# Kernel optimization log

Hardware: AMD Instinct MI355X
Metric: run time of the kernel (lower is better)

The kernel has to match this reference:

```python
import jax, jax.numpy as jnp
import numpy as np

N, E, IN, H, OUT = 100000, 1200000, 128, 64, 2
L = 3          # num GCN layers
EPS = 1e-5     # BatchNorm eps


def setup_inputs() -> dict:
    key = jax.random.key(0)
    ks = jax.random.split(key, 14)
    x = jax.random.normal(ks[0], (N, IN), dtype=jnp.float32)
    edge_index = jax.random.randint(ks[1], (2, E), 0, N, dtype=jnp.int64)
    # GCNConv weights (glorot-ish scale) and biases
    w0 = jax.random.normal(ks[2], (IN, H), dtype=jnp.float32) / np.float32(np.sqrt(IN))
    w1 = jax.random.normal(ks[3], (H, H), dtype=jnp.float32) / np.float32(np.sqrt(H))
    w2 = jax.random.normal(ks[4], (H, H), dtype=jnp.float32) / np.float32(np.sqrt(H))
    biases = jax.random.normal(ks[5], (L, H), dtype=jnp.float32) * 0.01
    # BatchNorm (eval mode): gamma, beta, running mean/var per layer
    gamma = jnp.ones((L, H), jnp.float32) + 0.1 * jax.random.normal(ks[6], (L, H), dtype=jnp.float32)
    beta = 0.1 * jax.random.normal(ks[7], (L, H), dtype=jnp.float32)
    run_mean = 0.1 * jax.random.normal(ks[8], (L, H), dtype=jnp.float32)
    run_var = 0.5 + jax.random.uniform(ks[9], (L, H), dtype=jnp.float32)  # strictly positive
    # classifier
    cls_w = jax.random.normal(ks[10], (H, OUT), dtype=jnp.float32) / np.float32(np.sqrt(H))
    cls_b = jnp.zeros((OUT,), jnp.float32)
    return {"x": x, "edge_index": edge_index, "w0": w0, "w1": w1, "w2": w2,
            "biases": biases, "gamma": gamma, "beta": beta,
            "run_mean": run_mean, "run_var": run_var,
            "cls_w": cls_w, "cls_b": cls_b}


def reference(x, edge_index, w0, w1, w2, biases, gamma, beta, run_mean, run_var, cls_w, cls_b):
    n = x.shape[0]
    loop = jnp.arange(n, dtype=edge_index.dtype)
    row = jnp.concatenate([edge_index[0], loop])  # source (with self-loops)
    col = jnp.concatenate([edge_index[1], loop])  # target (with self-loops)
    # symmetric normalization: D^{-1/2} (A+I) D^{-1/2}, degree on target index
    deg = jax.ops.segment_sum(jnp.ones(row.shape, x.dtype), col, num_segments=n)
    dinv = jnp.where(deg > 0, jax.lax.rsqrt(deg), 0.0)
    norm = dinv[row] * dinv[col]  # [E+N]

    h = x
    for l, w in enumerate((w0, w1, w2)):
        h = h @ w                                                   # [N,H]
        msg = norm[:, None] * h[row]                                # gather + scale [E+N,H]
        h = jax.ops.segment_sum(msg, col, num_segments=n) + biases[l]
        # BatchNorm1d (eval) + ReLU
        scale = gamma[l] * jax.lax.rsqrt(run_var[l] + EPS)
        h = jax.nn.relu((h - run_mean[l]) * scale + beta[l])
        # dropout is identity in eval mode
    return h @ cls_w + cls_b  # [N, OUT]
```

## Files before the change

### kernel.cpp

```cpp
#include <hip/hip_runtime.h>
#include <hip/hip_fp16.h>

#define EPS 1e-5f
#define ABITS 8
#define NBKT_MAX 512
#define ACHUNK 2048
#define BCAP 4096
#define BCSR 6144
#define CSHIFT 13
#define NCHUNK 16

typedef _Float16 half8 __attribute__((ext_vector_type(8)));
typedef float floatx4 __attribute__((ext_vector_type(4)));


__global__ __launch_bounds__(256) void bucketA_kernel(const int* __restrict__ ei, int E,
                                                      int* __restrict__ bucket_fill, unsigned* __restrict__ tmp) {
    __shared__ int2 edg[ACHUNK];
    __shared__ int hist[NBKT_MAX], lbase[NBKT_MAX], lcur[NBKT_MAX];
    int t = threadIdx.x;
    for (int i = t; i < NBKT_MAX; i += 256) { hist[i] = 0; lcur[i] = 0; }
    __syncthreads();
    int e0 = blockIdx.x * ACHUNK;
    int e1 = e0 + ACHUNK; if (e1 > E) e1 = E;
    int ne = e1 - e0;
    for (int idx = t; idx < ne; idx += 256) {
        int r = ei[e0 + idx], c = ei[E + e0 + idx];
        edg[idx] = make_int2(r, c);
        atomicAdd(&hist[c >> ABITS], 1);
    }
    __syncthreads();
    for (int i = t; i < NBKT_MAX; i += 256) {
        int h = hist[i];
        if (h) lbase[i] = atomicAdd(&bucket_fill[i], h);
    }
    __syncthreads();
    for (int idx = t; idx < ne; idx += 256) {
        int2 e = edg[idx];
        int b = e.y >> ABITS;
        int l = atomicAdd(&lcur[b], 1);
        tmp[(size_t)b * BCAP + lbase[b] + l] = ((unsigned)(e.y & 255) << 17) | (unsigned)e.x;
    }
}

__global__ __launch_bounds__(256) void bucketB_kernel(const unsigned* __restrict__ tmp,
                                                      const int* __restrict__ bucket_fill,
                                                      int2* __restrict__ rowse, float* __restrict__ dinv,
                                                      int* __restrict__ csr, int* __restrict__ perm, int n) {
    __shared__ unsigned edg[BCAP];
    __shared__ int cnt2[256 * NCHUNK];
    __shared__ int wsum[4];
    __shared__ int ccnt[16], cbaseS[16];
    int b = blockIdx.x, t = threadIdx.x;
    int lane = t & 63, wv = t >> 6;
    int n0 = b << ABITS;
    int cntN = n - n0; if (cntN > 256) cntN = 256;
    int ne = bucket_fill[b]; if (ne > BCAP) ne = BCAP;
    int base = b * BCAP;
    int cbase = b * BCSR;
    if (t < 16) ccnt[t] = 0;
    for (int i = t; i < 256 * NCHUNK; i += 256) cnt2[i] = 0;
    for (int idx = t; idx < ne; idx += 256) edg[idx] = tmp[(size_t)base + idx];
    __syncthreads();
    for (int idx = t; idx < ne; idx += 256) {
        unsigned e = edg[idx];
        int dstOff = e >> 17, src = e & 0x1FFFF;
        atomicAdd(&cnt2[dstOff * NCHUNK + (src >> CSHIFT)], 1);
    }
    __syncthreads();
    int c0 = 0;
#pragma unroll
    for (int c = 0; c < NCHUNK; ++c) c0 += cnt2[t * NCHUNK + c];
    int k0c = (c0 + 7) >> 3; if (k0c > 15) k0c = 15;
    int rank0 = 0;
    if (t < cntN) rank0 = atomicAdd(&ccnt[k0c], 1);
    int p0 = (c0 + 7) & ~7;
    int v = p0;
#pragma unroll
    for (int off = 1; off < 64; off <<= 1) {
        int u = __shfl_up(v, off);
        if (lane >= off) v += u;
    }
    if (lane == 63) wsum[wv] = v;
    __syncthreads();
    int addv = 0;
    for (int j = 0; j < wv; ++j) addv += wsum[j];
    int excl = v + addv - p0;
    int st0 = cbase + excl;
    if (t < cntN) {
        rowse[n0 + t] = make_int2(st0, st0 + c0);
        dinv[n0 + t] = rsqrtf((float)(c0 + 1));
        for (int j = c0; j < p0; ++j) csr[st0 + j] = n0 + t;
    }
    int run = st0;
#pragma unroll
    for (int c = 0; c < NCHUNK; ++c) {
        int vv = cnt2[t * NCHUNK + c];
        cnt2[t * NCHUNK + c] = run;
        run += vv;
    }
    if (t < 16) {
        int sacc = 0;
        for (int j = 0; j < t; ++j) sacc += ccnt[j];
        cbaseS[t] = sacc;
    }
    __syncthreads();
    if (t < cntN) perm[n0 + cbaseS[k0c] + rank0] = n0 + t;
    for (int idx = t; idx < ne; idx += 256) {
        unsigned e = edg[idx];
        int dstOff = e >> 17, src = e & 0x1FFFF;
        int key = dstOff * NCHUNK + (src >> CSHIFT);
        int pos = atomicAdd(&cnt2[key], 1);
        csr[pos] = src;
    }
}


template <int K, typename TIN>
__global__ __launch_bounds__(256) void gemm_kernel(const TIN* __restrict__ A, const float* __restrict__ W,
                                                   const float* __restrict__ dinv, __half* __restrict__ out, int n) {
    const int KP = K + 8;
    __shared__ _Float16 Ah[64 * (K + 8)];
    __shared__ _Float16 Wt[64 * (K + 8)];
    int tid = threadIdx.x;

    for (int idx = tid; idx < K * 64; idx += 256) {
        int k = idx >> 6, c = idx & 63;
        Wt[c * KP + k] = (_Float16)W[idx];
    }
    int row0 = blockIdx.x * 64;
    const TIN* Ab = A + (size_t)row0 * K;
    int limit = (n - row0) * K; if (limit > 64 * K) limit = 64 * K;

    if constexpr (sizeof(TIN) == 4) {
        for (int f = tid * 4; f < 64 * K; f += 1024) {
            float4 v = make_float4(0.f, 0.f, 0.f, 0.f);
            if (f + 3 < limit) {
                v = *(const float4*)((const float*)Ab + f);
            } else {
                if (f + 0 < limit) v.x = ((const float*)Ab)[f + 0];
                if (f + 1 < limit) v.y = ((const float*)Ab)[f + 1];
                if (f + 2 < limit) v.z = ((const float*)Ab)[f + 2];
            }
            int row = f / K, k = f % K;
            _Float16* dst = Ah + row * KP + k;
            dst[0] = (_Float16)v.x; dst[1] = (_Float16)v.y;
            dst[2] = (_Float16)v.z; dst[3] = (_Float16)v.w;
        }
    } else {
        for (int f = tid * 8; f < 64 * K; f += 2048) {
            uint4 v = make_uint4(0, 0, 0, 0);
            if (f + 7 < limit) {
                v = *(const uint4*)((const __half*)Ab + f);
            } else {
                const __half* hp = (const __half*)Ab;
                __half tmp8[8];
                for (int j = 0; j < 8; ++j) tmp8[j] = (f + j < limit) ? hp[f + j] : __half(0);
                v = *(const uint4*)tmp8;
            }
            int row = f / K, k = f % K;
            *(uint4*)(Ah + row * KP + k) = v;
        }
    }
    __syncthreads();

    int w = tid >> 6, lane = tid & 63;
    int m = lane & 15, quad = lane >> 4;
    const _Float16* Aw = Ah + (size_t)(w * 16 + m) * KP + quad * 8;
    const _Float16* Bw = Wt + (size_t)m * KP + quad * 8;

    floatx4 acc0 = {0.f, 0.f, 0.f, 0.f}, acc1 = acc0, acc2 = acc0, acc3 = acc0;
    for (int k0 = 0; k0 < K; k0 += 32) {
        half8 a  = *(const half8*)(Aw + k0);
        half8 b0 = *(const half8*)(Bw + 0 * 16 * KP + k0);
        half8 b1 = *(const half8*)(Bw + 1 * 16 * KP + k0);
        half8 b2 = *(const half8*)(Bw + 2 * 16 * KP + k0);
        half8 b3 = *(const half8*)(Bw + 3 * 16 * KP + k0);
        acc0 = __builtin_amdgcn_mfma_f32_16x16x32_f16(a, b0, acc0, 0, 0, 0);
        acc1 = __builtin_amdgcn_mfma_f32_16x16x32_f16(a, b1, acc1, 0, 0, 0);
        acc2 = __builtin_amdgcn_mfma_f32_16x16x32_f16(a, b2, acc2, 0, 0, 0);
        acc3 = __builtin_amdgcn_mfma_f32_16x16x32_f16(a, b3, acc3, 0, 0, 0);
    }

    int rbase = row0 + w * 16 + quad * 4;
#pragma unroll
    for (int r = 0; r < 4; ++r) {
        int row = rbase + r;
        if (row < n) {
            float dv = dinv[row];
            __half* o = out + (size_t)row * 64 + m;
            o[0]  = __float2half(acc0[r] * dv);
            o[16] = __float2half(acc1[r] * dv);
            o[32] = __float2half(acc2[r] * dv);
            o[48] = __float2half(acc3[r] * dv);
        }
    }
}


__device__ __forceinline__ void agg_add8(float4& lo, float4& hi, uint4 raw) {
    float2 p0 = __half22float2(*(const __half2*)&raw.x);
    float2 p1 = __half22float2(*(const __half2*)&raw.y);
    float2 p2 = __half22float2(*(const __half2*)&raw.z);
    float2 p3 = __half22float2(*(const __half2*)&raw.w);
    lo.x += p0.x; lo.y += p0.y; lo.z += p1.x; lo.w += p1.y;
    hi.x += p2.x; hi.y += p2.y; hi.z += p3.x; hi.w += p3.y;
}

__device__ __forceinline__ void agg_core(const __half* __restrict__ t, const float* __restrict__ dinv,
                                         const int2* __restrict__ rowse, const int* __restrict__ csr,
                                         const float* __restrict__ bias, const float* __restrict__ gamma,
                                         const float* __restrict__ beta, const float* __restrict__ mean,
                                         const float* __restrict__ var,
                                         int i, int fl, float4& resL, float4& resH, float& di) {
    uint4 self = *(const uint4*)(t + (size_t)i * 64 + fl * 8);

    float4 lo = make_float4(0.f, 0.f, 0.f, 0.f);
    float4 hi = make_float4(0.f, 0.f, 0.f, 0.f);

    int2 se = rowse[i];
    int deg = se.y - se.x;
    int padEnd = se.x + ((deg + 7) & ~7);
    for (int e = se.x; e < padEnd; e += 8) {
        int s0 = csr[e + 0], s1 = csr[e + 1], s2 = csr[e + 2], s3 = csr[e + 3];
        int s4 = csr[e + 4], s5 = csr[e + 5], s6 = csr[e + 6], s7 = csr[e + 7];
        uint4 r0 = *(const uint4*)(t + (size_t)s0 * 64 + fl * 8);
        uint4 r1 = *(const uint4*)(t + (size_t)s1 * 64 + fl * 8);
        uint4 r2 = *(const uint4*)(t + (size_t)s2 * 64 + fl * 8);
        uint4 r3 = *(const uint4*)(t + (size_t)s3 * 64 + fl * 8);
        uint4 r4 = *(const uint4*)(t + (size_t)s4 * 64 + fl * 8);
        uint4 r5 = *(const uint4*)(t + (size_t)s5 * 64 + fl * 8);
        uint4 r6 = *(const uint4*)(t + (size_t)s6 * 64 + fl * 8);
        uint4 r7 = *(const uint4*)(t + (size_t)s7 * 64 + fl * 8);
        agg_add8(lo, hi, r0); agg_add8(lo, hi, r1); agg_add8(lo, hi, r2); agg_add8(lo, hi, r3);
        agg_add8(lo, hi, r4); agg_add8(lo, hi, r5); agg_add8(lo, hi, r6); agg_add8(lo, hi, r7);
    }

    float coef = 1.0f - (float)(padEnd - se.y);
    {
        float2 p0 = __half22float2(*(const __half2*)&self.x);
        float2 p1 = __half22float2(*(const __half2*)&self.y);
        float2 p2 = __half22float2(*(const __half2*)&self.z);
        float2 p3 = __half22float2(*(const __half2*)&self.w);
        lo.x += coef * p0.x; lo.y += coef * p0.y; lo.z += coef * p1.x; lo.w += coef * p1.y;
        hi.x += coef * p2.x; hi.y += coef * p2.y; hi.z += coef * p3.x; hi.w += coef * p3.y;
    }

    di = dinv[i];
    lo.x *= di; lo.y *= di; lo.z *= di; lo.w *= di;
    hi.x *= di; hi.y *= di; hi.z *= di; hi.w *= di;

    float4 bbL = ((const float4*)bias)[2 * fl],  bbH = ((const float4*)bias)[2 * fl + 1];
    float4 ggL = ((const float4*)gamma)[2 * fl], ggH = ((const float4*)gamma)[2 * fl + 1];
    float4 beL = ((const float4*)beta)[2 * fl],  beH = ((const float4*)beta)[2 * fl + 1];
    float4 mmL = ((const float4*)mean)[2 * fl],  mmH = ((const float4*)mean)[2 * fl + 1];
    float4 vvL = ((const float4*)var)[2 * fl],   vvH = ((const float4*)var)[2 * fl + 1];
    resL.x = fmaxf((lo.x + bbL.x - mmL.x) * (ggL.x * rsqrtf(vvL.x + EPS)) + beL.x, 0.f);
    resL.y = fmaxf((lo.y + bbL.y - mmL.y) * (ggL.y * rsqrtf(vvL.y + EPS)) + beL.y, 0.f);
    resL.z = fmaxf((lo.z + bbL.z - mmL.z) * (ggL.z * rsqrtf(vvL.z + EPS)) + beL.z, 0.f);
    resL.w = fmaxf((lo.w + bbL.w - mmL.w) * (ggL.w * rsqrtf(vvL.w + EPS)) + beL.w, 0.f);
    resH.x = fmaxf((hi.x + bbH.x - mmH.x) * (ggH.x * rsqrtf(vvH.x + EPS)) + beH.x, 0.f);
    resH.y = fmaxf((hi.y + bbH.y - mmH.y) * (ggH.y * rsqrtf(vvH.y + EPS)) + beH.y, 0.f);
    resH.z = fmaxf((hi.z + bbH.z - mmH.z) * (ggH.z * rsqrtf(vvH.z + EPS)) + beH.z, 0.f);
    resH.w = fmaxf((hi.w + bbH.w - mmH.w) * (ggH.w * rsqrtf(vvH.w + EPS)) + beH.w, 0.f);
}

__global__ __launch_bounds__(256, 4) void agg_gemm_kernel(
        const __half* __restrict__ t, const float* __restrict__ dinv,
        const int2* __restrict__ rowse, const int* __restrict__ csr,
        const int* __restrict__ perm,
        const float* __restrict__ bias, const float* __restrict__ gamma,
        const float* __restrict__ beta, const float* __restrict__ mean,
        const float* __restrict__ var,
        const float* __restrict__ W,
        __half* __restrict__ tout, int n) {
    const int KP = 72;
    __shared__ _Float16 Ah[32 * 72];
    __shared__ _Float16 Wt[64 * 72];
    __shared__ int   nidS[32];
    __shared__ float dvS[32];

    int tid = threadIdx.x;
    for (int idx = tid; idx < 64 * 64; idx += 256) {
        int k = idx >> 6, c = idx & 63;
        Wt[c * KP + k] = (_Float16)W[idx];
    }

    int wave = tid >> 6, lane = tid & 63;
    int g = lane >> 3, fl = lane & 7;
    int slotInBlk = wave * 8 + g;
    int slot = blockIdx.x * 32 + slotInBlk;
    bool act = slot < n;

    if (act) {
        int i = perm[slot];
        float4 resL, resH; float di;
        agg_core(t, dinv, rowse, csr, bias, gamma, beta, mean, var, i, fl, resL, resH, di);
        __half2 h0 = __floats2half2_rn(resL.x, resL.y);
        __half2 h1 = __floats2half2_rn(resL.z, resL.w);
        __half2 h2 = __floats2half2_rn(resH.x, resH.y);
        __half2 h3 = __floats2half2_rn(resH.z, resH.w);
        uint4 pk;
        pk.x = *(unsigned*)&h0; pk.y = *(unsigned*)&h1;
        pk.z = *(unsigned*)&h2; pk.w = *(unsigned*)&h3;
        *(uint4*)(Ah + slotInBlk * KP + fl * 8) = pk;
        if (fl == 0) { nidS[slotInBlk] = i; dvS[slotInBlk] = di; }
    } else {
        uint4 z = make_uint4(0, 0, 0, 0);
        *(uint4*)(Ah + slotInBlk * KP + fl * 8) = z;
        if (fl == 0) { nidS[slotInBlk] = 0; dvS[slotInBlk] = 0.f; }
    }
    __syncthreads();

    int m = lane & 15, quad = lane >> 4;
    int mrow = (wave & 1) * 16;
    int c0 = (wave >> 1) * 32;
    const _Float16* Aw = Ah + (mrow + m) * KP + quad * 8;
    const _Float16* Bw = Wt + (c0 + m) * KP + quad * 8;

    floatx4 acc0 = {0.f, 0.f, 0.f, 0.f}, acc1 = acc0;
#pragma unroll
    for (int k0 = 0; k0 < 64; k0 += 32) {
        half8 a  = *(const half8*)(Aw + k0);
        half8 b0 = *(const half8*)(Bw + k0);
        half8 b1 = *(const half8*)(Bw + 16 * KP + k0);
        acc0 = __builtin_amdgcn_mfma_f32_16x16x32_f16(a, b0, acc0, 0, 0, 0);
        acc1 = __builtin_amdgcn_mfma_f32_16x16x32_f16(a, b1, acc1, 0, 0, 0);
    }
    __syncthreads();

#pragma unroll
    for (int r = 0; r < 4; ++r) {
        int row = mrow + quad * 4 + r;
        float dv = dvS[row];
        Ah[row * KP + c0 + m]      = (_Float16)(acc0[r] * dv);
        Ah[row * KP + c0 + 16 + m] = (_Float16)(acc1[r] * dv);
    }
    __syncthreads();

    if (act) {
        int node = nidS[slotInBlk];
        uint4 v = *(const uint4*)(Ah + slotInBlk * KP + fl * 8);
        *(uint4*)(tout + (size_t)node * 64 + fl * 8) = v;
    }
}

__global__ __launch_bounds__(256, 4) void agg_cls_kernel(
        const __half* __restrict__ t, const float* __restrict__ dinv,
        const int2* __restrict__ rowse, const int* __restrict__ csr,
        const int* __restrict__ perm,
        const float* __restrict__ bias, const float* __restrict__ gamma,
        const float* __restrict__ beta, const float* __restrict__ mean,
        const float* __restrict__ var,
        float* __restrict__ fout,
        const float* __restrict__ cls_w, const float* __restrict__ cls_b,
        int n) {
    int wave = threadIdx.x >> 6;
    int lane = threadIdx.x & 63;
    int g = lane >> 3;
    int fl = lane & 7;
    int slot = (blockIdx.x * (blockDim.x >> 6) + wave) * 8 + g;
    if (slot >= n) return;
    int i = perm[slot];

    float4 resL, resH; float di;
    agg_core(t, dinv, rowse, csr, bias, gamma, beta, mean, var, i, fl, resL, resH, di);

    const float4* cw = (const float4*)cls_w;
    float4 cwA = cw[4 * fl + 0], cwB = cw[4 * fl + 1], cwC = cw[4 * fl + 2], cwD = cw[4 * fl + 3];
    float c0 = resL.x * cwA.x + resL.y * cwA.z + resL.z * cwB.x + resL.w * cwB.z
             + resH.x * cwC.x + resH.y * cwC.z + resH.z * cwD.x + resH.w * cwD.z;
    float c1 = resL.x * cwA.y + resL.y * cwA.w + resL.z * cwB.y + resL.w * cwB.w
             + resH.x * cwC.y + resH.y * cwC.w + resH.z * cwD.y + resH.w * cwD.w;
    for (int off = 4; off > 0; off >>= 1) {
        c0 += __shfl_xor(c0, off);
        c1 += __shfl_xor(c1, off);
    }
    if (fl == 0) {
        fout[(size_t)i * 2 + 0] = c0 + cls_b[0];
        fout[(size_t)i * 2 + 1] = c1 + cls_b[1];
    }
}


extern "C" void kernel_launch(void* const* d_in, const int* in_sizes, int n_in,
                              void* d_out, int out_size, void* d_ws, size_t ws_size,
                              hipStream_t stream) {
    const float* x      = (const float*)d_in[0];
    const int*   ei     = (const int*)d_in[1];
    const float* w0     = (const float*)d_in[2];
    const float* w1     = (const float*)d_in[3];
    const float* w2     = (const float*)d_in[4];
    const float* biases = (const float*)d_in[5];
    const float* gamma  = (const float*)d_in[6];
    const float* beta   = (const float*)d_in[7];
    const float* rmean  = (const float*)d_in[8];
    const float* rvar   = (const float*)d_in[9];
    const float* cls_w  = (const float*)d_in[10];
    const float* cls_b  = (const float*)d_in[11];
    float* out = (float*)d_out;

    const int IN = 128, H = 64;
    const int N = in_sizes[0] / IN;
    const int E = in_sizes[1] / 2;

    char* p = (char*)d_ws;
    auto carve = [&](size_t bytes) { void* q = (void*)p; p += (bytes + 255) & ~(size_t)255; return q; };
    float* dinv    = (float*)carve((size_t)N * 4);
    int2*  rowse   = (int2*)carve((size_t)N * 8);
    int*   bucket_fill = (int*)carve((size_t)NBKT_MAX * 4);
    int*   perm    = (int*)carve((size_t)N * 4);
    unsigned* tmp  = (unsigned*)carve((size_t)NBKT_MAX * BCAP * 4);
    int*   csr     = (int*)carve((size_t)NBKT_MAX * BCSR * 4);
    __half* tA     = (__half*)carve((size_t)N * H * 2);
    __half* tB     = (__half*)carve((size_t)N * H * 2);

    int nbuckets = (N + (1 << ABITS) - 1) >> ABITS;
    int na = (E + ACHUNK - 1) / ACHUNK;

    hipMemsetAsync(bucket_fill, 0, (size_t)NBKT_MAX * 4, stream);
    bucketA_kernel<<<na, 256, 0, stream>>>(ei, E, bucket_fill, tmp);
    bucketB_kernel<<<nbuckets, 256, 0, stream>>>(tmp, bucket_fill, rowse, dinv, csr, perm, N);

    int gemm_grid = (N + 63) / 64;
    int agg_grid  = (N + 31) / 32;

    gemm_kernel<128, float><<<gemm_grid, 256, 0, stream>>>(x, w0, dinv, tA, N);
    agg_gemm_kernel<<<agg_grid, 256, 0, stream>>>(tA, dinv, rowse, csr, perm,
        biases + 0, gamma + 0, beta + 0, rmean + 0, rvar + 0, w1, tB, N);
    agg_gemm_kernel<<<agg_grid, 256, 0, stream>>>(tB, dinv, rowse, csr, perm,
        biases + H, gamma + H, beta + H, rmean + H, rvar + H, w2, tA, N);
    agg_cls_kernel<<<agg_grid, 256, 0, stream>>>(tA, dinv, rowse, csr, perm,
        biases + 2 * H, gamma + 2 * H, beta + 2 * H, rmean + 2 * H, rvar + 2 * H,
        out, cls_w, cls_b, N);
}
```

Before: 250.3 us.

## Merge all GCN stages into one persistent cooperative kernel with grid syncs

Replaces the six separate kernel launches (two bucketing passes, input GEMM, two aggregate+GEMM layers, final aggregate+classifier) with a single cooperative persistent kernel. Blocks loop over tiles within each phase and separate the phases with grid.sync, using one dynamic shared-memory buffer carved per phase. This removes per-launch overhead and the gaps between kernels. In exchange, occupancy is capped by the largest shared-memory phase, each block's loop adds extra __syncthreads, and every grid-wide barrier waits for the slowest block.

```diff
diff --git a/kernel.cpp b/kernel.cpp
--- a/kernel.cpp
+++ b/kernel.cpp
@@ -1,5 +1,8 @@
 #include <hip/hip_runtime.h>
 #include <hip/hip_fp16.h>
+#include <hip/hip_cooperative_groups.h>
+
+namespace cg = cooperative_groups;
 
 #define EPS 1e-5f
 #define ABITS 8
@@ -9,58 +12,72 @@
 #define BCSR 6144
 #define CSHIFT 13
 #define NCHUNK 16
+#define SMEM_BYTES 34816
 
 typedef _Float16 half8 __attribute__((ext_vector_type(8)));
 typedef float floatx4 __attribute__((ext_vector_type(4)));
 
-
-__global__ __launch_bounds__(256) void bucketA_kernel(const int* __restrict__ ei, int E,
-                                                      int* __restrict__ bucket_fill, unsigned* __restrict__ tmp) {
-    __shared__ int2 edg[ACHUNK];
-    __shared__ int hist[NBKT_MAX], lbase[NBKT_MAX], lcur[NBKT_MAX];
+struct GcnParams {
+    const float* x; const int* ei;
+    const float* w0; const float* w1; const float* w2;
+    const float* biases; const float* gamma; const float* beta;
+    const float* rmean; const float* rvar;
+    const float* cls_w; const float* cls_b;
+    float* out;
+    float* dinv; int2* rowse; int* bucket_fill; int* perm;
+    unsigned* tmp; int* csr; __half* tA; __half* tB;
+    int N, E, na, nbuckets, gtiles, atiles;
+};
+
+
+__device__ __forceinline__ void bucketA_body(char* smem, const GcnParams& P, int chunk) {
+    int2* edg  = (int2*)smem;
+    int* hist  = (int*)(smem + 16384);
+    int* lbase = (int*)(smem + 18432);
+    int* lcur  = (int*)(smem + 20480);
     int t = threadIdx.x;
     for (int i = t; i < NBKT_MAX; i += 256) { hist[i] = 0; lcur[i] = 0; }
     __syncthreads();
-    int e0 = blockIdx.x * ACHUNK;
-    int e1 = e0 + ACHUNK; if (e1 > E) e1 = E;
+    int e0 = chunk * ACHUNK;
+    int e1 = e0 + ACHUNK; if (e1 > P.E) e1 = P.E;
     int ne = e1 - e0;
     for (int idx = t; idx < ne; idx += 256) {
-        int r = ei[e0 + idx], c = ei[E + e0 + idx];
+        int r = P.ei[e0 + idx], c = P.ei[P.E + e0 + idx];
         edg[idx] = make_int2(r, c);
         atomicAdd(&hist[c >> ABITS], 1);
     }
     __syncthreads();
     for (int i = t; i < NBKT_MAX; i += 256) {
         int h = hist[i];
-        if (h) lbase[i] = atomicAdd(&bucket_fill[i], h);
+        if (h) lbase[i] = atomicAdd(&P.bucket_fill[i], h);
     }
     __syncthreads();
     for (int idx = t; idx < ne; idx += 256) {
         int2 e = edg[idx];
         int b = e.y >> ABITS;
         int l = atomicAdd(&lcur[b], 1);
-        tmp[(size_t)b * BCAP + lbase[b] + l] = ((unsigned)(e.y & 255) << 17) | (unsigned)e.x;
-    }
-}
-
-__global__ __launch_bounds__(256) void bucketB_kernel(const unsigned* __restrict__ tmp,
-                                                      const int* __restrict__ bucket_fill,
-                                                      int2* __restrict__ rowse, float* __restrict__ dinv,
-                                                      int* __restrict__ csr, int* __restrict__ perm, int n) {
-    __shared__ unsigned edg[BCAP];
-    __shared__ int cnt2[256 * NCHUNK];
-    __shared__ int wsum[4];
-    __shared__ int ccnt[16], cbaseS[16];
-    int b = blockIdx.x, t = threadIdx.x;
+        P.tmp[(size_t)b * BCAP + lbase[b] + l] = ((unsigned)(e.y & 255) << 17) | (unsigned)e.x;
+    }
+    __syncthreads();
+}
+
+
+__device__ __forceinline__ void bucketB_body(char* smem, const GcnParams& P, int b) {
+    unsigned* edg = (unsigned*)smem;
+    int* cnt2   = (int*)(smem + 16384);
+    int* wsum   = (int*)(smem + 32768);
+    int* ccnt   = (int*)(smem + 32784);
+    int* cbaseS = (int*)(smem + 32848);
+    int t = threadIdx.x;
     int lane = t & 63, wv = t >> 6;
     int n0 = b << ABITS;
-    int cntN = n - n0; if (cntN > 256) cntN = 256;
-    int ne = bucket_fill[b]; if (ne > BCAP) ne = BCAP;
+    int cntN = P.N - n0; if (cntN > 256) cntN = 256;
+    int ne = P.bucket_fill[b]; if (ne > BCAP) ne = BCAP;
     int base = b * BCAP;
     int cbase = b * BCSR;
     if (t < 16) ccnt[t] = 0;
     for (int i = t; i < 256 * NCHUNK; i += 256) cnt2[i] = 0;
-    for (int idx = t; idx < ne; idx += 256) edg[idx] = tmp[(size_t)base + idx];
+    for (int idx = t; idx < ne; idx += 256) edg[idx] = P.tmp[(size_t)base + idx];
     __syncthreads();
     for (int idx = t; idx < ne; idx += 256) {
         unsigned e = edg[idx];
@@ -88,9 +105,9 @@
     int excl = v + addv - p0;
     int st0 = cbase + excl;
     if (t < cntN) {
-        rowse[n0 + t] = make_int2(st0, st0 + c0);
-        dinv[n0 + t] = rsqrtf((float)(c0 + 1));
-        for (int j = c0; j < p0; ++j) csr[st0 + j] = n0 + t;
+        P.rowse[n0 + t] = make_int2(st0, st0 + c0);
+        P.dinv[n0 + t] = rsqrtf((float)(c0 + 1));
+        for (int j = c0; j < p0; ++j) P.csr[st0 + j] = n0 + t;
     }
     int run = st0;
 #pragma unroll
@@ -105,95 +122,78 @@
         cbaseS[t] = sacc;
     }
     __syncthreads();
-    if (t < cntN) perm[n0 + cbaseS[k0c] + rank0] = n0 + t;
+    if (t < cntN) P.perm[n0 + cbaseS[k0c] + rank0] = n0 + t;
     for (int idx = t; idx < ne; idx += 256) {
         unsigned e = edg[idx];
         int dstOff = e >> 17, src = e & 0x1FFFF;
         int key = dstOff * NCHUNK + (src >> CSHIFT);
         int pos = atomicAdd(&cnt2[key], 1);
-        csr[pos] = src;
-    }
-}
-
-
-template <int K, typename TIN>
-__global__ __launch_bounds__(256) void gemm_kernel(const TIN* __restrict__ A, const float* __restrict__ W,
-                                                   const float* __restrict__ dinv, __half* __restrict__ out, int n) {
-    const int KP = K + 8;
-    __shared__ _Float16 Ah[64 * (K + 8)];
-    __shared__ _Float16 Wt[64 * (K + 8)];
+        P.csr[pos] = src;
+    }
+    __syncthreads();
+}
+
+
+__device__ __forceinline__ void gemm_phase(char* smem, const GcnParams& P, int bid, int gdim) {
+    const int K = 128, KP = 136;
+    _Float16* Ah = (_Float16*)smem;
+    _Float16* Wt = (_Float16*)(smem + 17408);
     int tid = threadIdx.x;
-
     for (int idx = tid; idx < K * 64; idx += 256) {
         int k = idx >> 6, c = idx & 63;
-        Wt[c * KP + k] = (_Float16)W[idx];
-    }
-    int row0 = blockIdx.x * 64;
-    const TIN* Ab = A + (size_t)row0 * K;
-    int limit = (n - row0) * K; if (limit > 64 * K) limit = 64 * K;
-
-    if constexpr (sizeof(TIN) == 4) {
+        Wt[c * KP + k] = (_Float16)P.w0[idx];
+    }
+    __syncthreads();
+    int w = tid >> 6, lane = tid & 63;
+    int m = lane & 15, quad = lane >> 4;
+    for (int tile = bid; tile < P.gtiles; tile += gdim) {
+        int row0 = tile * 64;
+        const float* Ab = P.x + (size_t)row0 * K;
+        int limit = (P.N - row0) * K; if (limit > 64 * K) limit = 64 * K;
         for (int f = tid * 4; f < 64 * K; f += 1024) {
             float4 v = make_float4(0.f, 0.f, 0.f, 0.f);
             if (f + 3 < limit) {
-                v = *(const float4*)((const float*)Ab + f);
+                v = *(const float4*)(Ab + f);
             } else {
-                if (f + 0 < limit) v.x = ((const float*)Ab)[f + 0];
-                if (f + 1 < limit) v.y = ((const float*)Ab)[f + 1];
-                if (f + 2 < limit) v.z = ((const float*)Ab)[f + 2];
+                if (f + 0 < limit) v.x = Ab[f + 0];
+                if (f + 1 < limit) v.y = Ab[f + 1];
+                if (f + 2 < limit) v.z = Ab[f + 2];
             }
-            int row = f / K, k = f % K;
+            int row = f >> 7, k = f & 127;
             _Float16* dst = Ah + row * KP + k;
             dst[0] = (_Float16)v.x; dst[1] = (_Float16)v.y;
             dst[2] = (_Float16)v.z; dst[3] = (_Float16)v.w;
         }
-    } else {
-        for (int f = tid * 8; f < 64 * K; f += 2048) {
-            uint4 v = make_uint4(0, 0, 0, 0);
-            if (f + 7 < limit) {
-                v = *(const uint4*)((const __half*)Ab + f);
-            } else {
-                const __half* hp = (const __half*)Ab;
-                __half tmp8[8];
-                for (int j = 0; j < 8; ++j) tmp8[j] = (f + j < limit) ? hp[f + j] : __half(0);
-                v = *(const uint4*)tmp8;
+        __syncthreads();
+        const _Float16* Aw = Ah + (size_t)(w * 16 + m) * KP + quad * 8;
+        const _Float16* Bw = Wt + (size_t)m * KP + quad * 8;
+        floatx4 acc0 = {0.f, 0.f, 0.f, 0.f}, acc1 = acc0, acc2 = acc0, acc3 = acc0;
+#pragma unroll
+        for (int k0 = 0; k0 < K; k0 += 32) {
+            half8 a  = *(const half8*)(Aw + k0);
+            half8 b0 = *(const half8*)(Bw + 0 * 16 * KP + k0);
+            half8 b1 = *(const half8*)(Bw + 1 * 16 * KP + k0);
+            half8 b2 = *(const half8*)(Bw + 2 * 16 * KP + k0);
+            half8 b3 = *(const half8*)(Bw + 3 * 16 * KP + k0);
+            acc0 = __builtin_amdgcn_mfma_f32_16x16x32_f16(a, b0, acc0, 0, 0, 0);
+            acc1 = __builtin_amdgcn_mfma_f32_16x16x32_f16(a, b1, acc1, 0, 0, 0);
+            acc2 = __builtin_amdgcn_mfma_f32_16x16x32_f16(a, b2, acc2, 0, 0, 0);
+            acc3 = __builtin_amdgcn_mfma_f32_16x16x32_f16(a, b3, acc3, 0, 0, 0);
+        }
+        int rbase = row0 + w * 16 + quad * 4;
+#pragma unroll
+        for (int r = 0; r < 4; ++r) {
+            int row = rbase + r;
+            if (row < P.N) {
+                float dv = P.dinv[row];
+                __half* o = P.tA + (size_t)row * 64 + m;
+                o[0]  = __float2half(acc0[r] * dv);
+                o[16] = __float2half(acc1[r] * dv);
+                o[32] = __float2half(acc2[r] * dv);
+                o[48] = __float2half(acc3[r] * dv);
             }
-            int row = f / K, k = f % K;
-            *(uint4*)(Ah + row * KP + k) = v;
-        }
-    }
-    __syncthreads();
-
-    int w = tid >> 6, lane = tid & 63;
-    int m = lane & 15, quad = lane >> 4;
-    const _Float16* Aw = Ah + (size_t)(w * 16 + m) * KP + quad * 8;
-    const _Float16* Bw = Wt + (size_t)m * KP + quad * 8;
-
-    floatx4 acc0 = {0.f, 0.f, 0.f, 0.f}, acc1 = acc0, acc2 = acc0, acc3 = acc0;
-    for (int k0 = 0; k0 < K; k0 += 32) {
-        half8 a  = *(const half8*)(Aw + k0);
-        half8 b0 = *(const half8*)(Bw + 0 * 16 * KP + k0);
-        half8 b1 = *(const half8*)(Bw + 1 * 16 * KP + k0);
-        half8 b2 = *(const half8*)(Bw + 2 * 16 * KP + k0);
-        half8 b3 = *(const half8*)(Bw + 3 * 16 * KP + k0);
-        acc0 = __builtin_amdgcn_mfma_f32_16x16x32_f16(a, b0, acc0, 0, 0, 0);
-        acc1 = __builtin_amdgcn_mfma_f32_16x16x32_f16(a, b1, acc1, 0, 0, 0);
-        acc2 = __builtin_amdgcn_mfma_f32_16x16x32_f16(a, b2, acc2, 0, 0, 0);
-        acc3 = __builtin_amdgcn_mfma_f32_16x16x32_f16(a, b3, acc3, 0, 0, 0);
-    }
-
-    int rbase = row0 + w * 16 + quad * 4;
-#pragma unroll
-    for (int r = 0; r < 4; ++r) {
-        int row = rbase + r;
-        if (row < n) {
-            float dv = dinv[row];
-            __half* o = out + (size_t)row * 64 + m;
-            o[0]  = __float2half(acc0[r] * dv);
-            o[16] = __float2half(acc1[r] * dv);
-            o[32] = __float2half(acc2[r] * dv);
-            o[48] = __float2half(acc3[r] * dv);
-        }
+        }
+        __syncthreads();
     }
 }
 
@@ -265,172 +265,198 @@
     resH.w = fmaxf((hi.w + bbH.w - mmH.w) * (ggH.w * rsqrtf(vvH.w + EPS)) + beH.w, 0.f);
 }
 
-__global__ __launch_bounds__(256, 4) void agg_gemm_kernel(
-        const __half* __restrict__ t, const float* __restrict__ dinv,
-        const int2* __restrict__ rowse, const int* __restrict__ csr,
-        const int* __restrict__ perm,
-        const float* __restrict__ bias, const float* __restrict__ gamma,
-        const float* __restrict__ beta, const float* __restrict__ mean,
-        const float* __restrict__ var,
-        const float* __restrict__ W,
-        __half* __restrict__ tout, int n) {
+
+__device__ __forceinline__ void agg_gemm_phase(char* smem, const GcnParams& P,
+        const __half* tin, const float* W,
+        const float* bias, const float* gamma, const float* beta,
+        const float* mean, const float* var,
+        __half* tout, int bid, int gdim) {
     const int KP = 72;
-    __shared__ _Float16 Ah[32 * 72];
-    __shared__ _Float16 Wt[64 * 72];
-    __shared__ int   nidS[32];
-    __shared__ float dvS[32];
-
+    _Float16* Ah = (_Float16*)smem;
+    _Float16* Wt = (_Float16*)(smem + 4608);
+    int*   nidS  = (int*)(smem + 13824);
+    float* dvS   = (float*)(smem + 13952);
     int tid = threadIdx.x;
     for (int idx = tid; idx < 64 * 64; idx += 256) {
         int k = idx >> 6, c = idx & 63;
         Wt[c * KP + k] = (_Float16)W[idx];
     }
-
+    __syncthreads();
     int wave = tid >> 6, lane = tid & 63;
     int g = lane >> 3, fl = lane & 7;
     int slotInBlk = wave * 8 + g;
-    int slot = blockIdx.x * 32 + slotInBlk;
-    bool act = slot < n;
-
-    if (act) {
-        int i = perm[slot];
-        float4 resL, resH; float di;
-        agg_core(t, dinv, rowse, csr, bias, gamma, beta, mean, var, i, fl, resL, resH, di);
-        __half2 h0 = __floats2half2_rn(resL.x, resL.y);
-        __half2 h1 = __floats2half2_rn(resL.z, resL.w);
-        __half2 h2 = __floats2half2_rn(resH.x, resH.y);
-        __half2 h3 = __floats2half2_rn(resH.z, resH.w);
-        uint4 pk;
-        pk.x = *(unsigned*)&h0; pk.y = *(unsigned*)&h1;
-        pk.z = *(unsigned*)&h2; pk.w = *(unsigned*)&h3;
-        *(uint4*)(Ah + slotInBlk * KP + fl * 8) = pk;
-        if (fl == 0) { nidS[slotInBlk] = i; dvS[slotInBlk] = di; }
-    } else {
-        uint4 z = make_uint4(0, 0, 0, 0);
-        *(uint4*)(Ah + slotInBlk * KP + fl * 8) = z;
-        if (fl == 0) { nidS[slotInBlk] = 0; dvS[slotInBlk] = 0.f; }
-    }
-    __syncthreads();
-
     int m = lane & 15, quad = lane >> 4;
     int mrow = (wave & 1) * 16;
     int c0 = (wave >> 1) * 32;
-    const _Float16* Aw = Ah + (mrow + m) * KP + quad * 8;
-    const _Float16* Bw = Wt + (c0 + m) * KP + quad * 8;
-
-    floatx4 acc0 = {0.f, 0.f, 0.f, 0.f}, acc1 = acc0;
-#pragma unroll
-    for (int k0 = 0; k0 < 64; k0 += 32) {
-        half8 a  = *(const half8*)(Aw + k0);
-        half8 b0 = *(const half8*)(Bw + k0);
-        half8 b1 = *(const half8*)(Bw + 16 * KP + k0);
-        acc0 = __builtin_amdgcn_mfma_f32_16x16x32_f16(a, b0, acc0, 0, 0, 0);
-        acc1 = __builtin_amdgcn_mfma_f32_16x16x32_f16(a, b1, acc1, 0, 0, 0);
-    }
-    __syncthreads();
-
-#pragma unroll
-    for (int r = 0; r < 4; ++r) {
-        int row = mrow + quad * 4 + r;
-        float dv = dvS[row];
-        Ah[row * KP + c0 + m]      = (_Float16)(acc0[r] * dv);
-        Ah[row * KP + c0 + 16 + m] = (_Float16)(acc1[r] * dv);
-    }
-    __syncthreads();
-
-    if (act) {
-        int node = nidS[slotInBlk];
-        uint4 v = *(const uint4*)(Ah + slotInBlk * KP + fl * 8);
-        *(uint4*)(tout + (size_t)node * 64 + fl * 8) = v;
-    }
-}
-
-__global__ __launch_bounds__(256, 4) void agg_cls_kernel(
-        const __half* __restrict__ t, const float* __restrict__ dinv,
-        const int2* __restrict__ rowse, const int* __restrict__ csr,
-        const int* __restrict__ perm,
-        const float* __restrict__ bias, const float* __restrict__ gamma,
-        const float* __restrict__ beta, const float* __restrict__ mean,
-        const float* __restrict__ var,
-        float* __restrict__ fout,
-        const float* __restrict__ cls_w, const float* __restrict__ cls_b,
-        int n) {
-    int wave = threadIdx.x >> 6;
-    int lane = threadIdx.x & 63;
-    int g = lane >> 3;
-    int fl = lane & 7;
-    int slot = (blockIdx.x * (blockDim.x >> 6) + wave) * 8 + g;
-    if (slot >= n) return;
-    int i = perm[slot];
-
-    float4 resL, resH; float di;
-    agg_core(t, dinv, rowse, csr, bias, gamma, beta, mean, var, i, fl, resL, resH, di);
-
-    const float4* cw = (const float4*)cls_w;
-    float4 cwA = cw[4 * fl + 0], cwB = cw[4 * fl + 1], cwC = cw[4 * fl + 2], cwD = cw[4 * fl + 3];
-    float c0 = resL.x * cwA.x + resL.y * cwA.z + resL.z * cwB.x + resL.w * cwB.z
-             + resH.x * cwC.x + resH.y * cwC.z + resH.z * cwD.x + resH.w * cwD.z;
-    float c1 = resL.x * cwA.y + resL.y * cwA.w + resL.z * cwB.y + resL.w * cwB.w
-             + resH.x * cwC.y + resH.y * cwC.w + resH.z * cwD.y + resH.w * cwD.w;
-    for (int off = 4; off > 0; off >>= 1) {
-        c0 += __shfl_xor(c0, off);
-        c1 += __shfl_xor(c1, off);
-    }
-    if (fl == 0) {
-        fout[(size_t)i * 2 + 0] = c0 + cls_b[0];
-        fout[(size_t)i * 2 + 1] = c1 + cls_b[1];
-    }
+    for (int tile = bid; tile < P.atiles; tile += gdim) {
+        int slot = tile * 32 + slotInBlk;
+        bool act = slot < P.N;
+        if (act) {
+            int i = P.perm[slot];
+            float4 resL, resH; float di;
+            agg_core(tin, P.dinv, P.rowse, P.csr, bias, gamma, beta, mean, var, i, fl, resL, resH, di);
+            __half2 h0 = __floats2half2_rn(resL.x, resL.y);
+            __half2 h1 = __floats2half2_rn(resL.z, resL.w);
+            __half2 h2 = __floats2half2_rn(resH.x, resH.y);
+            __half2 h3 = __floats2half2_rn(resH.z, resH.w);
+            uint4 pk;
+            pk.x = *(unsigned*)&h0; pk.y = *(unsigned*)&h1;
+            pk.z = *(unsigned*)&h2; pk.w = *(unsigned*)&h3;
+            *(uint4*)(Ah + slotInBlk * KP + fl * 8) = pk;
+            if (fl == 0) { nidS[slotInBlk] = i; dvS[slotInBlk] = di; }
+        } else {
+            uint4 z = make_uint4(0, 0, 0, 0);
+            *(uint4*)(Ah + slotInBlk * KP + fl * 8) = z;
+            if (fl == 0) { nidS[slotInBlk] = 0; dvS[slotInBlk] = 0.f; }
+        }
+        __syncthreads();
+
+        const _Float16* Aw = Ah + (mrow + m) * KP + quad * 8;
+        const _Float16* Bw = Wt + (c0 + m) * KP + quad * 8;
+        floatx4 acc0 = {0.f, 0.f, 0.f, 0.f}, acc1 = acc0;
+#pragma unroll
+        for (int k0 = 0; k0 < 64; k0 += 32) {
+            half8 a  = *(const half8*)(Aw + k0);
+            half8 b0 = *(const half8*)(Bw + k0);
+            half8 b1 = *(const half8*)(Bw + 16 * KP + k0);
+            acc0 = __builtin_amdgcn_mfma_f32_16x16x32_f16(a, b0, acc0, 0, 0, 0);
+            acc1 = __builtin_amdgcn_mfma_f32_16x16x32_f16(a, b1, acc1, 0, 0, 0);
+        }
+        __syncthreads();
+
+#pragma unroll
+        for (int r = 0; r < 4; ++r) {
+            int row = mrow + quad * 4 + r;
+            float dv = dvS[row];
+            Ah[row * KP + c0 + m]      = (_Float16)(acc0[r] * dv);
+            Ah[row * KP + c0 + 16 + m] = (_Float16)(acc1[r] * dv);
+        }
+        __syncthreads();
+
+        if (act) {
+            int node = nidS[slotInBlk];
+            uint4 v = *(const uint4*)(Ah + slotInBlk * KP + fl * 8);
+            *(uint4*)(tout + (size_t)node * 64 + fl * 8) = v;
+        }
+        __syncthreads();
+    }
+}
+
+
+__device__ __forceinline__ void agg_cls_phase(const GcnParams& P, int bid, int gdim) {
+    int tid = threadIdx.x;
+    int wave = tid >> 6, lane = tid & 63;
+    int g = lane >> 3, fl = lane & 7;
+    int slotInBlk = wave * 8 + g;
+    const float* bias  = P.biases + 128;
+    const float* gamma = P.gamma + 128;
+    const float* beta  = P.beta + 128;
+    const float* mean  = P.rmean + 128;
+    const float* var   = P.rvar + 128;
+    for (int tile = bid; tile < P.atiles; tile += gdim) {
+        int slot = tile * 32 + slotInBlk;
+        if (slot >= P.N) continue;
+        int i = P.perm[slot];
+        float4 resL, resH; float di;
+        agg_core(P.tA, P.dinv, P.rowse, P.csr, bias, gamma, beta, mean, var, i, fl, resL, resH, di);
+        const float4* cw = (const float4*)P.cls_w;
+        float4 cwA = cw[4 * fl + 0], cwB = cw[4 * fl + 1], cwC = cw[4 * fl + 2], cwD = cw[4 * fl + 3];
+        float c0 = resL.x * cwA.x + resL.y * cwA.z + resL.z * cwB.x + resL.w * cwB.z
+                 + resH.x * cwC.x + resH.y * cwC.z + resH.z * cwD.x + resH.w * cwD.z;
+        float c1 = resL.x * cwA.y + resL.y * cwA.w + resL.z * cwB.y + resL.w * cwB.w
+                 + resH.x * cwC.y + resH.y * cwC.w + resH.z * cwD.y + resH.w * cwD.w;
+        for (int off = 4; off > 0; off >>= 1) {
+            c0 += __shfl_xor(c0, off);
+            c1 += __shfl_xor(c1, off);
+        }
+        if (fl == 0) {
+            P.out[(size_t)i * 2 + 0] = c0 + P.cls_b[0];
+            P.out[(size_t)i * 2 + 1] = c1 + P.cls_b[1];
+        }
+    }
+}
+
+
+__global__ __launch_bounds__(256, 4) void gcn_merged(GcnParams P) {
+    extern __shared__ char smem[];
+    cg::grid_group grid = cg::this_grid();
+    int bid = blockIdx.x, gdim = gridDim.x;
+
+    for (int c = bid; c < P.na; c += gdim) bucketA_body(smem, P, c);
+    grid.sync();
+    for (int b = bid; b < P.nbuckets; b += gdim) bucketB_body(smem, P, b);
+    grid.sync();
+    gemm_phase(smem, P, bid, gdim);
+    grid.sync();
+#pragma unroll 1
+    for (int l = 0; l < 2; ++l) {
+        const __half* tin = l ? P.tB : P.tA;
+        __half* tout      = l ? P.tA : P.tB;
+        const float* W    = l ? P.w2 : P.w1;
+        int off = l * 64;
+        agg_gemm_phase(smem, P, tin, W, P.biases + off, P.gamma + off, P.beta + off,
+                       P.rmean + off, P.rvar + off, tout, bid, gdim);
+        grid.sync();
+    }
+    agg_cls_phase(P, bid, gdim);
 }
 
 
 extern "C" void kernel_launch(void* const* d_in, const int* in_sizes, int n_in,
                               void* d_out, int out_size, void* d_ws, size_t ws_size,
                               hipStream_t stream) {
-    const float* x      = (const float*)d_in[0];
-    const int*   ei     = (const int*)d_in[1];
-    const float* w0     = (const float*)d_in[2];
-    const float* w1     = (const float*)d_in[3];
-    const float* w2     = (const float*)d_in[4];
-    const float* biases = (const float*)d_in[5];
-    const float* gamma  = (const float*)d_in[6];
-    const float* beta   = (const float*)d_in[7];
-    const float* rmean  = (const float*)d_in[8];
-    const float* rvar   = (const float*)d_in[9];
-    const float* cls_w  = (const float*)d_in[10];
-    const float* cls_b  = (const float*)d_in[11];
-    float* out = (float*)d_out;
-
-    const int IN = 128, H = 64;
-    const int N = in_sizes[0] / IN;
-    const int E = in_sizes[1] / 2;
+    GcnParams P;
+    P.x      = (const float*)d_in[0];
+    P.ei     = (const int*)d_in[1];
+    P.w0     = (const float*)d_in[2];
+    P.w1     = (const float*)d_in[3];
+    P.w2     = (const float*)d_in[4];
+    P.biases = (const float*)d_in[5];
+    P.gamma  = (const float*)d_in[6];
+    P.beta   = (const float*)d_in[7];
+    P.rmean  = (const float*)d_in[8];
+    P.rvar   = (const float*)d_in[9];
+    P.cls_w  = (const float*)d_in[10];
+    P.cls_b  = (const float*)d_in[11];
+    P.out    = (float*)d_out;
+
+    const int IN_ = 128, H = 64;
+    int N = in_sizes[0] / IN_;
+    int E = in_sizes[1] / 2;
 
     char* p = (char*)d_ws;
     auto carve = [&](size_t bytes) { void* q = (void*)p; p += (bytes + 255) & ~(size_t)255; return q; };
-    float* dinv    = (float*)carve((size_t)N * 4);
-    int2*  rowse   = (int2*)carve((size_t)N * 8);
-    int*   bucket_fill = (int*)carve((size_t)NBKT_MAX * 4);
-    int*   perm    = (int*)carve((size_t)N * 4);
-    unsigned* tmp  = (unsigned*)carve((size_t)NBKT_MAX * BCAP * 4);
-    int*   csr     = (int*)carve((size_t)NBKT_MAX * BCSR * 4);
-    __half* tA     = (__half*)carve((size_t)N * H * 2);
-    __half* tB     = (__half*)carve((size_t)N * H * 2);
-
-    int nbuckets = (N + (1 << ABITS) - 1) >> ABITS;
-    int na = (E + ACHUNK - 1) / ACHUNK;
-
-    hipMemsetAsync(bucket_fill, 0, (size_t)NBKT_MAX * 4, stream);
-    bucketA_kernel<<<na, 256, 0, stream>>>(ei, E, bucket_fill, tmp);
-    bucketB_kernel<<<nbuckets, 256, 0, stream>>>(tmp, bucket_fill, rowse, dinv, csr, perm, N);
-
-    int gemm_grid = (N + 63) / 64;
-    int agg_grid  = (N + 31) / 32;
-
-    gemm_kernel<128, float><<<gemm_grid, 256, 0, stream>>>(x, w0, dinv, tA, N);
-    agg_gemm_kernel<<<agg_grid, 256, 0, stream>>>(tA, dinv, rowse, csr, perm,
-        biases + 0, gamma + 0, beta + 0, rmean + 0, rvar + 0, w1, tB, N);
-    agg_gemm_kernel<<<agg_grid, 256, 0, stream>>>(tB, dinv, rowse, csr, perm,
-        biases + H, gamma + H, beta + H, rmean + H, rvar + H, w2, tA, N);
-    agg_cls_kernel<<<agg_grid, 256, 0, stream>>>(tA, dinv, rowse, csr, perm,
-        biases + 2 * H, gamma + 2 * H, beta + 2 * H, rmean + 2 * H, rvar + 2 * H,
-        out, cls_w, cls_b, N);
-}
+    P.dinv        = (float*)carve((size_t)N * 4);
+    P.rowse       = (int2*)carve((size_t)N * 8);
+    P.bucket_fill = (int*)carve((size_t)NBKT_MAX * 4);
+    P.perm        = (int*)carve((size_t)N * 4);
+    P.tmp         = (unsigned*)carve((size_t)NBKT_MAX * BCAP * 4);
+    P.csr         = (int*)carve((size_t)NBKT_MAX * BCSR * 4);
+    P.tA          = (__half*)carve((size_t)N * H * 2);
+    P.tB          = (__half*)carve((size_t)N * H * 2);
+
+    P.N = N; P.E = E;
+    P.na = (E + ACHUNK - 1) / ACHUNK;
+    P.nbuckets = (N + 255) >> 8;
+    P.gtiles = (N + 63) / 64;
+    P.atiles = (N + 31) / 32;
+
+    hipMemsetAsync(P.bucket_fill, 0, (size_t)NBKT_MAX * 4, stream);
+
+    static int s_grid = 0;
+    if (s_grid == 0) {
+        int maxb = 0;
+        hipOccupancyMaxActiveBlocksPerMultiprocessor(&maxb, (const void*)gcn_merged, 256, SMEM_BYTES);
+        if (maxb < 1) maxb = 1;
+        int dev = 0;
+        hipGetDevice(&dev);
+        int nCU = 0;
+        hipDeviceGetAttribute(&nCU, hipDeviceAttributeMultiprocessorCount, dev);
+        if (nCU <= 0) nCU = 256;
+        s_grid = maxb * nCU;
+    }
+
+    void* kargs[] = { (void*)&P };
+    hipLaunchCooperativeKernel((const void*)gcn_merged, dim3(s_grid), dim3(256), kargs,
+                               SMEM_BYTES, stream);
+}
```

Measured after the change: 612.3 us. 145% more time.
